# Kernel optimization log

Measured on AMD Instinct MI355X. Metric: run time of the kernel, lower is better.

## Reference

```python
import jax, jax.numpy as jnp
import numpy as np

B, R, L_, K_, U_, E = 16, 32, 64, 16, 4, 64  # batch, realizations, APs, users, antennas, embed dim
C2 = 2 * U_                                   # input_dim_2 == output_dim == 2U
EPS = 1e-5


def _uniform(key, shape, fan_out, fan_in):
    # matches torch init: U(-ini, ini) with ini = sqrt(3/(out*in))
    ini = float(np.sqrt(3.0 / (fan_out * fan_in)))
    return jax.random.uniform(key, shape, jnp.float32, -ini, ini)


def setup_inputs() -> dict:
    key = jax.random.key(0)
    ks = jax.random.split(key, 12)
    return {
        "Hhat_real": jax.random.normal(ks[0], (B, R, L_, K_, U_), jnp.float32),
        "Hhat_imag": jax.random.normal(ks[1], (B, R, L_, K_, U_), jnp.float32),
        # layer 0 (hidden, out=E) -- note P3/P5 exist in torch but are unused in forward
        "P1_0": _uniform(ks[2], (E, E), E, E),
        "P2_0": _uniform(ks[3], (E, E), E, E),
        "P4_0": _uniform(ks[4], (E, C2), E, C2),
        "g0": jnp.ones((E,), jnp.float32),
        "b0": jnp.zeros((E,), jnp.float32),
        # layer 1 (hidden, out=E)
        "P1_1": _uniform(ks[5], (E, E), E, E),
        "P2_1": _uniform(ks[6], (E, E), E, E),
        "P4_1": _uniform(ks[7], (E, C2), E, C2),
        "g1": jnp.ones((E,), jnp.float32),
        "b1": jnp.zeros((E,), jnp.float32),
        # layer 2 (output, out=2U, no BN / no ReLU)
        "P1_2": _uniform(ks[8], (C2, E), C2, E),
        "P2_2": _uniform(ks[9], (C2, E), C2, E),
        "P4_2": _uniform(ks[10], (C2, C2), C2, C2),
        "nbrOfRealizations": R,
        "L": L_,
        "K": K_,
        "U": U_,
    }


def _layer(A, H, P1, P2, P4, gamma, beta, is_last):
    # A: [BR, C1, L, K], H: [BR, C2, L, K]
    A1 = jnp.einsum('oc,bclk->bolk', P1, A)
    A2 = jnp.einsum('oc,bcl->bol', P2, A.mean(-1))[:, :, :, None]   # mean over K
    A3 = jnp.einsum('oc,bck->bok', P2, A.mean(-2))[:, :, None, :]   # mean over L
    A4 = jnp.einsum('oc,bcl->bol', P4, H.mean(-1))[:, :, :, None]
    A5 = jnp.einsum('oc,bck->bok', P4, H.mean(-2))[:, :, None, :]
    out = 2 * A1 + 2 * A2 + 2 * A3 + 0.1 * A4 + 0.1 * A5
    if is_last:
        return out
    out = jax.nn.relu(out)
    # BatchNorm2d, training mode: biased variance over (batch, L, K)
    mu = out.mean((0, 2, 3), keepdims=True)
    var = ((out - mu) ** 2).mean((0, 2, 3), keepdims=True)
    return (out - mu) / jnp.sqrt(var + EPS) * gamma[None, :, None, None] + beta[None, :, None, None]


def reference(Hhat_real, Hhat_imag, P1_0, P2_0, P4_0, g0, b0,
              P1_1, P2_1, P4_1, g1, b1, P1_2, P2_2, P4_2,
              nbrOfRealizations, L, K, U):
    batch = Hhat_real.shape[0]
    BR = batch * nbrOfRealizations
    # [B,R,L,K,U] -> [BR,U,L,K] (real / imag channels), concat -> [BR, 2U, L, K]
    Hr = Hhat_real.reshape(BR, L, K, U).transpose(0, 3, 1, 2)
    Hi = Hhat_imag.reshape(BR, L, K, U).transpose(0, 3, 1, 2)
    Hup = jnp.concatenate([Hr, Hi], axis=1)
    A = jnp.zeros((BR, E, L, K), jnp.float32)  # V_AP_updated init
    A = _layer(A, Hup, P1_0, P2_0, P4_0, g0, b0, False)
    A = _layer(A, Hup, P1_1, P2_1, P4_1, g1, b1, False)
    V = _layer(A, Hup, P1_2, P2_2, P4_2, None, None, True)  # [BR, 2U, L, K]
    V = V.reshape(BR, 2, U, L, K)
    F1 = jnp.transpose(V[:, 0], (0, 2, 3, 1))  # [BR, L, K, U]
    F2 = jnp.transpose(V[:, 1], (0, 2, 3, 1))
    norm = jnp.sqrt((F1 ** 2).sum(-1) + (F2 ** 2).sum(-1))[..., None]
    Fhat = (F1 + 1j * F2) / norm
    return Fhat.reshape(batch, nbrOfRealizations, L, K, U)
```

## Files before the change

kernel.cpp:

```cpp
#include <hip/hip_runtime.h>
#include <math.h>

#define BRR 512
#define LLL 64
#define KKK 16
#define EEE 64
#define CC2 8
#define PPP 1024
#define BN_EPS 1e-5f
#define NSTRIPE 16

__device__ __forceinline__ float relu_f(float v){ return v>0.f?v:0.f; }
__device__ __forceinline__ int lds_row(int r){ return r*68 + (((r>>3)&7)<<2); }

#define OFF_HBL  0u
#define OFF_HBK  262144u
#define OFF_Y0   327680u
#define OFF_X1   851968u
#define OFF_Y1   2949120u
#define OFF_X2   3473408u
#define OFF_Y2   3735552u
#define OFF_M1L  3801088u
#define OFF_M1K  5898240u
#define OFF_SUM0 6422528u
#define OFF_SSQ0 6423552u
#define OFF_SUM1 6424576u
#define OFF_SSQ1 6425600u
#define OFF_S0   6426624u
#define OFF_T0   6426688u
#define OFF_S1   6426752u
#define OFF_T1   6426816u
#define WS_FLOATS 6426880u
#define OFF_M1KB 6426880u
#define OFF_T1S  6951168u
#define WS_BIG   40505600u

__global__ void k_zero(float4* __restrict__ p, int n4){
  int t = blockIdx.x*256 + threadIdx.x;
  if (t < n4) p[t] = make_float4(0.f,0.f,0.f,0.f);
}

__global__ __launch_bounds__(256) void k_prep(const float* __restrict__ Hr,
                                              const float* __restrict__ Hi,
                                              const float* __restrict__ P40,
                                              float* __restrict__ ws){
  __shared__ float sm[9344];
  int b = blockIdx.x, tid = threadIdx.x;
  const float* hrg = Hr + (size_t)b*4096;
  const float* hig = Hi + (size_t)b*4096;
  for (int t=tid;t<4096;t+=256){ sm[t]=hrg[t]; sm[4096+t]=hig[t]; }
  for (int t=tid;t<512;t+=256){ int c=t&63,j=t>>6; sm[8192+j*64+c]=P40[c*8+j]; }
  __syncthreads();
  for (int t=tid;t<512;t+=256){ int l=t>>3,c2=t&7;
    const float* src=sm+((c2<4)?0:4096); int u=c2&3;
    float s=0.f;
    #pragma unroll
    for(int k=0;k<16;++k) s+=src[(l*16+k)*4+u];
    sm[8704+t]=s*(1.f/16.f); }
  for (int t=tid;t<128;t+=256){ int k=t>>3,c2=t&7;
    const float* src=sm+((c2<4)?0:4096); int u=c2&3;
    float s=0.f;
    for(int l=0;l<64;++l) s+=src[(l*16+k)*4+u];
    sm[9216+t]=s*(1.f/64.f); }
  __syncthreads();
  for (int t=tid;t<1024;t+=256){ int k=t>>6,c=t&63; float s=0.f;
    #pragma unroll
    for(int j=0;j<8;++j) s+=sm[8192+j*64+c]*sm[9216+k*8+j];
    sm[4096+t]=0.1f*s; }
  for (int t=tid;t<4096;t+=256){ int l=t>>6,c=t&63; float s=0.f;
    #pragma unroll
    for(int j=0;j<8;++j) s+=sm[8192+j*64+c]*sm[8704+l*8+j];
    sm[t]=0.1f*s; }
  __syncthreads();
  for (int t=tid;t<1024;t+=256){ int c=t&63; float yv=sm[4096+t]; float s=0.f;
    for(int l=0;l<64;++l) s+=relu_f(sm[l*64+c]+yv);
    sm[5120+t]=s*(1.f/64.f); }
  float ssum=0.f, ssq=0.f;
  for (int t=tid;t<4096;t+=256){ int c=t&63; float xv=sm[t]; float s=0.f;
    #pragma unroll
    for(int k=0;k<16;++k){ float v=relu_f(xv+sm[4096+k*64+c]); s+=v; ssq+=v*v; }
    ssum+=s;
    ws[OFF_X1+(size_t)b*4096+t]=s*(1.f/16.f); }
  __syncthreads();
  sm[6144+tid]=ssum; sm[6400+tid]=ssq;
  __syncthreads();
  if (tid<64){
    float ts =sm[6144+tid]+sm[6208+tid]+sm[6272+tid]+sm[6336+tid];
    float tss=sm[6400+tid]+sm[6464+tid]+sm[6528+tid]+sm[6592+tid];
    int stripe = b & (NSTRIPE-1);
    atomicAdd(&ws[OFF_SUM0+stripe*64+tid], ts);
    atomicAdd(&ws[OFF_SSQ0+stripe*64+tid], tss);
  }
  for (int t=tid;t<512;t+=256)  ws[OFF_HBL+(size_t)b*512+t]=sm[8704+t];
  for (int t=tid;t<128;t+=256)  ws[OFF_HBK+(size_t)b*128+t]=sm[9216+t];
  for (int t=tid;t<1024;t+=256) ws[OFF_Y0+(size_t)b*1024+t]=sm[4096+t];
  for (int t=tid;t<1024;t+=256) ws[OFF_Y1+(size_t)b*1024+t]=sm[5120+t];
  for (int t=tid;t<4096;t+=256) ws[OFF_M1L+(size_t)b*4096+t]=sm[t];
}

__global__ void k_bn(float* __restrict__ ws, const float* __restrict__ g_,
                     const float* __restrict__ b_, unsigned sumOff, unsigned outOff){
  int tid = threadIdx.x;
  if (tid < 64){
    float s=0.f, ss=0.f;
    for (int i=0;i<NSTRIPE;++i){ s+=ws[sumOff+i*64+tid]; ss+=ws[sumOff+1024+i*64+tid]; }
    const float invN = 1.0f/((float)BRR*LLL*KKK);
    float mu=s*invN, var=ss*invN-mu*mu;
    float sc = g_[tid]/sqrtf(var+BN_EPS);
    ws[outOff+tid]=sc;
    ws[outOff+64+tid]=b_[tid]-mu*sc;
  }
}

__global__ __launch_bounds__(256) void k_xy1(float* __restrict__ ws,
                                             const float* __restrict__ P21,
                                             const float* __restrict__ P41){
  __shared__ float wt[4096], p41[512], mrow[1024], hbs[128], s0l[64], t0l[64];
  int bx = blockIdx.x, tid = threadIdx.x;
  for (int t=tid;t<4096;t+=256) wt[t] = 2.0f*P21[(t&63)*64 + (t>>6)];
  for (int t=tid;t<512;t+=256)  p41[t] = P41[t];
  if (tid<64){ s0l[tid]=ws[OFF_S0+tid]; t0l[tid]=ws[OFF_T0+tid]; }
  bool isX = bx < 2048;
  int row0 = isX ? bx*16 : (bx-2048)*16;
  if (isX){
    for (int t=tid;t<1024;t+=256) mrow[t] = ws[OFF_X1+(size_t)row0*64+t];
    if (tid<128) hbs[tid] = ws[OFF_HBL+(size_t)row0*8+tid];
  } else {
    for (int t=tid;t<1024;t+=256) mrow[t] = ws[OFF_Y1+(size_t)row0*64+t];
    if (tid<128) hbs[tid] = ws[OFF_HBK+(size_t)row0*8+tid];
  }
  __syncthreads();
  for (int t=tid;t<1024;t+=256){ int c=t&63; mrow[t]=s0l[c]*mrow[t]+t0l[c]; }
  __syncthreads();
  int r4 = tid>>6, o = tid&63;
  #pragma unroll
  for (int rr=0;rr<4;++rr){
    int rl = rr*4 + r4;
    float s=0.f;
    for (int c=0;c<64;++c) s += wt[c*64+o]*mrow[rl*64+c];
    float s2=0.f;
    #pragma unroll
    for (int j=0;j<8;++j) s2 += p41[o*8+j]*hbs[rl*8+j];
    float res = s + 0.1f*s2;
    if (isX) ws[OFF_X1+(size_t)(row0+rl)*64+o] = res;
    else     ws[OFF_Y1+(size_t)(row0+rl)*64+o] = res;
  }
}

#define T_W1   0
#define T_X08  4384
#define T_Y0   4896
#define T_X1   5984
#define T_Y1   6496
#define T_S0   7520
#define T_T0   7584
#define T_P4T0 7648
#define T_HB8  8160
#define T_END  8224

__device__ void t1_tile(float* sm, const float* __restrict__ ws,
                        const float* __restrict__ P11, const float* __restrict__ P40,
                        int b, int pblk, int tid,
                        float acc[8][4], int og, int pg, int lloc, int c0){
  for (int t=tid;t<4096;t+=256){ int o=t>>6,c=t&63; sm[T_W1+lds_row(o)+c]=2.0f*P11[t]; }
  for (int t=tid;t<1024;t+=256){ int k=t>>6,c=t&63; sm[T_Y0+k*68+c]=ws[OFF_Y0+(size_t)b*1024+t]; }
  for (int t=tid;t<512;t+=256)  sm[T_X1+t]=ws[OFF_X1+((size_t)b*64+pblk*8)*64+t];
  for (int t=tid;t<1024;t+=256) sm[T_Y1+t]=ws[OFF_Y1+(size_t)b*1024+t];
  for (int t=tid;t<512;t+=256){ int c=t&63,j=t>>6; sm[T_P4T0+j*64+c]=P40[c*8+j]; }
  if (tid<64){ sm[T_S0+tid]=ws[OFF_S0+tid]; sm[T_T0+tid]=ws[OFF_T0+tid]; }
  else if (tid<128){ int t2=tid-64; sm[T_HB8+t2]=ws[OFF_HBL+((size_t)b*64+pblk*8)*8+t2]; }
  __syncthreads();
  for (int e=tid;e<512;e+=256){ int l=e>>6,c=e&63; float s=0.f;
    #pragma unroll
    for(int j=0;j<8;++j) s += sm[T_P4T0+j*64+c]*sm[T_HB8+l*8+j];
    sm[T_X08+e]=0.1f*s; }
  __syncthreads();
  {
    float xb[8];
    *(float4*)&xb[0] = *(const float4*)&sm[T_X1 + lloc*64 + c0];
    *(float4*)&xb[4] = *(const float4*)&sm[T_X1 + lloc*64 + c0 + 4];
    #pragma unroll
    for (int i=0;i<4;++i){
      int k=(pg&3)*4+i;
      float yb[8];
      *(float4*)&yb[0] = *(const float4*)&sm[T_Y1 + k*64 + c0];
      *(float4*)&yb[4] = *(const float4*)&sm[T_Y1 + k*64 + c0 + 4];
      #pragma unroll
      for (int j=0;j<8;++j) acc[j][i]=xb[j]+yb[j];
    }
  }
  #pragma unroll 4
  for (int c4=0;c4<16;++c4){
    float4 xr  = *(const float4*)&sm[T_X08 + lloc*64 + c4*4];
    float4 s0v = *(const float4*)&sm[T_S0 + c4*4];
    float4 t0v = *(const float4*)&sm[T_T0 + c4*4];
    float4 aa[4];
    #pragma unroll
    for (int i=0;i<4;++i){
      int k=(pg&3)*4+i;
      float4 yr = *(const float4*)&sm[T_Y0 + k*68 + c4*4];
      aa[i].x = s0v.x*relu_f(xr.x+yr.x)+t0v.x;
      aa[i].y = s0v.y*relu_f(xr.y+yr.y)+t0v.y;
      aa[i].z = s0v.z*relu_f(xr.z+yr.z)+t0v.z;
      aa[i].w = s0v.w*relu_f(xr.w+yr.w)+t0v.w;
    }
    #pragma unroll
    for (int j=0;j<8;++j){
      float4 w = *(const float4*)&sm[T_W1 + lds_row(c0+j) + c4*4];
      #pragma unroll
      for (int i=0;i<4;++i)
        acc[j][i] += w.x*aa[i].x + w.y*aa[i].y + w.z*aa[i].z + w.w*aa[i].w;
    }
  }
  #pragma unroll
  for (int j=0;j<8;++j)
    #pragma unroll
    for (int i=0;i<4;++i) acc[j][i] = relu_f(acc[j][i]);
}

#define PD_W1   0
#define PD_Y0   4384
#define PD_Y1   5472
#define PD_X1D  6496
#define PD_X08D 7520
#define PD_CT   8544
#define PD_S0   8608
#define PD_T0   8672
#define PD_TOT  8736

__global__ __launch_bounds__(256) void k_pass1f(float* __restrict__ ws,
                                                const float* __restrict__ P11){
  __shared__ float sm[PD_TOT];
  int b = blockIdx.x >> 1, h = blockIdx.x & 1;
  int pb0 = h*4;
  int tid=threadIdx.x;
  int og=tid&7, kg=(tid>>3)&3, lloc=tid>>5, c0=og*8, wv=tid>>6;
  for (int t4=tid;t4<1024;t4+=256){ int o=t4>>4,c=(t4&15)*4;
    float4 v = *(const float4*)&P11[o*64+c];
    v.x*=2.f; v.y*=2.f; v.z*=2.f; v.w*=2.f;
    *(float4*)&sm[PD_W1+lds_row(o)+c]=v; }
  for (int t4=tid;t4<256;t4+=256){
    float4 v = *(const float4*)&ws[OFF_Y0+(size_t)b*1024+t4*4];
    *(float4*)&sm[PD_Y0+(t4>>4)*68+((t4&15)*4)]=v; }
  for (int t4=tid;t4<256;t4+=256)
    *(float4*)&sm[PD_Y1+t4*4] = *(const float4*)&ws[OFF_Y1+(size_t)b*1024+t4*4];
  if (tid<64){ sm[PD_S0+tid]=ws[OFF_S0+tid]; sm[PD_T0+tid]=ws[OFF_T0+tid]; }
  {
    int po = tid>>7, idx = tid&127;
    float4 v1 = *(const float4*)&ws[OFF_X1 +((size_t)b*64+(pb0+po)*8)*64 + (size_t)idx*4];
    float4 v8 = *(const float4*)&ws[OFF_M1L+((size_t)b*64+(pb0+po)*8)*64 + (size_t)idx*4];
    *(float4*)&sm[PD_X1D  + po*512 + idx*4] = v1;
    *(float4*)&sm[PD_X08D + po*512 + idx*4] = v8;
  }
  __syncthreads();
  if (tid<64){
    float ct=0.f;
    for (int c=0;c<64;++c) ct += sm[PD_W1+lds_row(tid)+c]*sm[PD_T0+c];
    sm[PD_CT+tid]=ct;
  }
  __syncthreads();
  for (int t4=tid;t4<1024;t4+=256){ int o=t4>>4,c=(t4&15)*4;
    float4 w = *(float4*)&sm[PD_W1+lds_row(o)+c];
    float4 s = *(const float4*)&sm[PD_S0+c];
    w.x*=s.x; w.y*=s.y; w.z*=s.z; w.w*=s.w;
    *(float4*)&sm[PD_W1+lds_row(o)+c]=w; }
  float qsum[8], mk[8][4];
  #pragma unroll
  for (int j=0;j<8;++j){ qsum[j]=0.f;
    #pragma unroll
    for (int i=0;i<4;++i) mk[j][i]=0.f; }
  #pragma unroll 1
  for (int pr=0;pr<2;++pr){
    int pblkA = pb0 + 2*pr, pblkB = pblkA + 1;
    __syncthreads();
    float4 n1, n8;
    if (pr==0){
      int po = tid>>7, idx = tid&127, pn = pb0 + 2 + po;
      n1 = *(const float4*)&ws[OFF_X1 +((size_t)b*64+pn*8)*64 + (size_t)idx*4];
      n8 = *(const float4*)&ws[OFF_M1L+((size_t)b*64+pn*8)*64 + (size_t)idx*4];
    }
    float accA[8][4], accB[8][4];
    {
      float xbA[8], xbB[8], ctv[8];
      *(float4*)&xbA[0] = *(const float4*)&sm[PD_X1D       + lloc*64 + c0];
      *(float4*)&xbA[4] = *(const float4*)&sm[PD_X1D       + lloc*64 + c0 + 4];
      *(float4*)&xbB[0] = *(const float4*)&sm[PD_X1D + 512 + lloc*64 + c0];
      *(float4*)&xbB[4] = *(const float4*)&sm[PD_X1D + 512 + lloc*64 + c0 + 4];
      *(float4*)&ctv[0] = *(const float4*)&sm[PD_CT + c0];
      *(float4*)&ctv[4] = *(const float4*)&sm[PD_CT + c0 + 4];
      #pragma unroll
      for (int i=0;i<4;++i){
        int k=kg*4+i;
        float yb[8];
        *(float4*)&yb[0] = *(const float4*)&sm[PD_Y1 + k*64 + c0];
        *(float4*)&yb[4] = *(const float4*)&sm[PD_Y1 + k*64 + c0 + 4];
        #pragma unroll
        for (int j=0;j<8;++j){
          float base = yb[j]+ctv[j];
          accA[j][i]=xbA[j]+base;
          accB[j][i]=xbB[j]+base;
        }
      }
    }
    #pragma unroll 2
    for (int c4=0;c4<16;++c4){
      float4 xrA = *(const float4*)&sm[PD_X08D       + lloc*64 + c4*4];
      float4 xrB = *(const float4*)&sm[PD_X08D + 512 + lloc*64 + c4*4];
      float4 aaA[4], aaB[4];
      #pragma unroll
      for (int i=0;i<4;++i){
        int k=kg*4+i;
        float4 yr = *(const float4*)&sm[PD_Y0 + k*68 + c4*4];
        aaA[i].x = relu_f(xrA.x+yr.x); aaB[i].x = relu_f(xrB.x+yr.x);
        aaA[i].y = relu_f(xrA.y+yr.y); aaB[i].y = relu_f(xrB.y+yr.y);
        aaA[i].z = relu_f(xrA.z+yr.z); aaB[i].z = relu_f(xrB.z+yr.z);
        aaA[i].w = relu_f(xrA.w+yr.w); aaB[i].w = relu_f(xrB.w+yr.w);
      }
      #pragma unroll
      for (int j=0;j<8;++j){
        float4 w = *(const float4*)&sm[PD_W1 + lds_row(c0+j) + c4*4];
        #pragma unroll
        for (int i=0;i<4;++i){
          accA[j][i] += w.x*aaA[i].x + w.y*aaA[i].y + w.z*aaA[i].z + w.w*aaA[i].w;
          accB[j][i] += w.x*aaB[i].x + w.y*aaB[i].y + w.z*aaB[i].z + w.w*aaB[i].w;
        }
      }
    }
    #pragma unroll
    for (int j=0;j<8;++j)
      #pragma unroll
      for (int i=0;i<4;++i){
        accA[j][i] = relu_f(accA[j][i]);
        accB[j][i] = relu_f(accB[j][i]);
      }
    {
      size_t tbA = OFF_T1S + ((size_t)b*8 + pblkA)*8192 + (size_t)tid*4;
      size_t tbB = OFF_T1S + ((size_t)b*8 + pblkB)*8192 + (size_t)tid*4;
      #pragma unroll
      for (int j=0;j<8;++j){
        *(float4*)&ws[tbA + j*1024] =
          make_float4(accA[j][0],accA[j][1],accA[j][2],accA[j][3]);
        *(float4*)&ws[tbB + j*1024] =
          make_float4(accB[j][0],accB[j][1],accB[j][2],accB[j][3]);
      }
    }
    float sjA[8], sjB[8];
    #pragma unroll
    for (int j=0;j<8;++j){
      sjA[j]=accA[j][0]+accA[j][1]+accA[j][2]+accA[j][3];
      sjB[j]=accB[j][0]+accB[j][1]+accB[j][2]+accB[j][3];
      qsum[j]+=accA[j][0]*accA[j][0]+accA[j][1]*accA[j][1]+accA[j][2]*accA[j][2]+accA[j][3]*accA[j][3];
      qsum[j]+=accB[j][0]*accB[j][0]+accB[j][1]*accB[j][1]+accB[j][2]*accB[j][2]+accB[j][3]*accB[j][3];
      #pragma unroll
      for (int i=0;i<4;++i) mk[j][i]+=accA[j][i]+accB[j][i];
    }
    #pragma unroll
    for (int j=0;j<8;++j){
      float rA=sjA[j];
      rA += __shfl_xor(rA, 8, 64);
      rA += __shfl_xor(rA, 16, 64);
      sjA[j]=rA;
      float rB=sjB[j];
      rB += __shfl_xor(rB, 8, 64);
      rB += __shfl_xor(rB, 16, 64);
      sjB[j]=rB;
    }
    if (kg==0){
      const float inv16 = 1.f/16.f;
      size_t baseA = OFF_M1L + ((size_t)b*64 + pblkA*8 + lloc)*64 + c0;
      size_t baseB = OFF_M1L + ((size_t)b*64 + pblkB*8 + lloc)*64 + c0;
      *(float4*)&ws[baseA]   = make_float4(sjA[0]*inv16, sjA[1]*inv16, sjA[2]*inv16, sjA[3]*inv16);
      *(float4*)&ws[baseA+4] = make_float4(sjA[4]*inv16, sjA[5]*inv16, sjA[6]*inv16, sjA[7]*inv16);
      *(float4*)&ws[baseB]   = make_float4(sjB[0]*inv16, sjB[1]*inv16, sjB[2]*inv16, sjB[3]*inv16);
      *(float4*)&ws[baseB+4] = make_float4(sjB[4]*inv16, sjB[5]*inv16, sjB[6]*inv16, sjB[7]*inv16);
    }
    if (pr==0){
      __syncthreads();
      int po = tid>>7, idx = tid&127;
      *(float4*)&sm[PD_X1D  + po*512 + idx*4] = n1;
      *(float4*)&sm[PD_X08D + po*512 + idx*4] = n8;
    }
  }
  __syncthreads();
  #pragma unroll
  for (int j=0;j<8;++j){
    #pragma unroll
    for (int i=0;i<4;++i){
      float v = mk[j][i] + __shfl_xor(mk[j][i], 32, 64);
      if ((tid & 32)==0)
        sm[wv*1088 + (og*4+kg)*33 + i*8 + j] = v;
    }
  }
  {
    int pg = tid>>3;
    #pragma unroll
    for (int j=0;j<8;++j) sm[4384+(c0+j)*33+pg] = qsum[j];
  }
  __syncthreads();
  unsigned mko = h ? OFF_M1KB : OFF_M1K;
  float tsacc=0.f;
  #pragma unroll
  for (int r=0;r<4;++r){
    int e = tid + r*256;
    int k=e>>6, c=e&63;
    int a = ((c>>3)*4+(k>>2))*33 + (k&3)*8 + (c&7);
    float v = sm[a]+sm[1088+a]+sm[2176+a]+sm[3264+a];
    tsacc += v;
    ws[mko+(size_t)b*1024+e] = v*(1.f/64.f);
  }
  sm[6496 + (tid&63)*5 + wv] = tsacc;
  __syncthreads();
  if (tid<64){
    float ts  = sm[6496+tid*5+0]+sm[6496+tid*5+1]+sm[6496+tid*5+2]+sm[6496+tid*5+3];
    float tss = 0.f;
    for (int g=0; g<32; ++g) tss += sm[4384+tid*33+g];
    int stripe = b & (NSTRIPE-1);
    atomicAdd(&ws[OFF_SUM1+stripe*64+tid], ts);
    atomicAdd(&ws[OFF_SSQ1+stripe*64+tid], tss);
  }
}

#define MK_OFF 8224
__global__ __launch_bounds__(256) void k_pass1(float* __restrict__ ws,
                                               const float* __restrict__ P11,
                                               const float* __restrict__ P40){
  __shared__ float sm[12576];
  int b=blockIdx.x, tid=threadIdx.x;
  int og=tid&7, pg=tid>>3, lloc=pg>>2, kg=pg&3, c0=og*8, wv=tid>>6;
  for (int t=tid;t<4096;t+=256){ int o=t>>6,c=t&63; sm[T_W1+lds_row(o)+c]=2.0f*P11[t]; }
  for (int t=tid;t<1024;t+=256){ int k=t>>6,c=t&63; sm[T_Y0+k*68+c]=ws[OFF_Y0+(size_t)b*1024+t]; }
  for (int t=tid;t<1024;t+=256) sm[T_Y1+t]=ws[OFF_Y1+(size_t)b*1024+t];
  for (int t=tid;t<512;t+=256){ int c=t&63,j=t>>6; sm[T_P4T0+j*64+c]=P40[c*8+j]; }
  if (tid<64){ sm[T_S0+tid]=ws[OFF_S0+tid]; sm[T_T0+tid]=ws[OFF_T0+tid]; }
  for (int t=tid;t<4352;t+=256) sm[MK_OFF+t]=0.f;
  float qsum[8];
  #pragma unroll
  for (int j=0;j<8;++j) qsum[j]=0.f;
  #pragma unroll 1
  for (int pblk=0;pblk<8;++pblk){
    __syncthreads();
    for (int t=tid;t<512;t+=256) sm[T_X1+t]=ws[OFF_X1+((size_t)b*64+pblk*8)*64+t];
    if (tid<64) sm[T_HB8+tid]=ws[OFF_HBL+((size_t)b*64+pblk*8)*8+tid];
    __syncthreads();
    for (int e=tid;e<512;e+=256){ int l=e>>6,c=e&63; float s=0.f;
      #pragma unroll
      for(int j=0;j<8;++j) s += sm[T_P4T0+j*64+c]*sm[T_HB8+l*8+j];
      sm[T_X08+e]=0.1f*s; }
    __syncthreads();
    float acc[8][4];
    {
      float xb[8];
      *(float4*)&xb[0] = *(const float4*)&sm[T_X1 + lloc*64 + c0];
      *(float4*)&xb[4] = *(const float4*)&sm[T_X1 + lloc*64 + c0 + 4];
      #pragma unroll
      for (int i=0;i<4;++i){
        int k=kg*4+i;
        float yb[8];
        *(float4*)&yb[0] = *(const float4*)&sm[T_Y1 + k*64 + c0];
        *(float4*)&yb[4] = *(const float4*)&sm[T_Y1 + k*64 + c0 + 4];
        #pragma unroll
        for (int j=0;j<8;++j) acc[j][i]=xb[j]+yb[j];
      }
    }
    #pragma unroll 4
    for (int c4=0;c4<16;++c4){
      float4 xr  = *(const float4*)&sm[T_X08 + lloc*64 + c4*4];
      float4 s0v = *(const float4*)&sm[T_S0 + c4*4];
      float4 t0v = *(const float4*)&sm[T_T0 + c4*4];
      float4 aa[4];
      #pragma unroll
      for (int i=0;i<4;++i){
        int k=kg*4+i;
        float4 yr = *(const float4*)&sm[T_Y0 + k*68 + c4*4];
        aa[i].x = s0v.x*relu_f(xr.x+yr.x)+t0v.x;
        aa[i].y = s0v.y*relu_f(xr.y+yr.y)+t0v.y;
        aa[i].z = s0v.z*relu_f(xr.z+yr.z)+t0v.z;
        aa[i].w = s0v.w*relu_f(xr.w+yr.w)+t0v.w;
      }
      #pragma unroll
      for (int j=0;j<8;++j){
        float4 w = *(const float4*)&sm[T_W1 + lds_row(c0+j) + c4*4];
        #pragma unroll
        for (int i=0;i<4;++i)
          acc[j][i] += w.x*aa[i].x + w.y*aa[i].y + w.z*aa[i].z + w.w*aa[i].w;
      }
    }
    #pragma unroll
    for (int j=0;j<8;++j)
      #pragma unroll
      for (int i=0;i<4;++i) acc[j][i] = relu_f(acc[j][i]);
    float sj[8];
    #pragma unroll
    for (int j=0;j<8;++j){
      sj[j]=acc[j][0]+acc[j][1]+acc[j][2]+acc[j][3];
      qsum[j]+=acc[j][0]*acc[j][0]+acc[j][1]*acc[j][1]+acc[j][2]*acc[j][2]+acc[j][3]*acc[j][3];
    }
    #pragma unroll
    for (int j=0;j<8;++j){
      float r=sj[j];
      r += __shfl_xor(r, 8, 64);
      r += __shfl_xor(r, 16, 64);
      sj[j]=r;
    }
    if (kg==0){
      const float inv16 = 1.f/16.f;
      float4 v0 = make_float4(sj[0]*inv16, sj[1]*inv16, sj[2]*inv16, sj[3]*inv16);
      float4 v1 = make_float4(sj[4]*inv16, sj[5]*inv16, sj[6]*inv16, sj[7]*inv16);
      size_t base = OFF_M1L + ((size_t)b*64 + pblk*8 + lloc)*64 + c0;
      *(float4*)&ws[base]   = v0;
      *(float4*)&ws[base+4] = v1;
    }
    #pragma unroll
    for (int j=0;j<8;++j){
      #pragma unroll
      for (int i=0;i<4;++i){
        float v = acc[j][i] + __shfl_xor(acc[j][i], 32, 64);
        if ((tid & 32)==0)
          sm[MK_OFF + wv*1088 + (og*4+kg)*33 + i*8 + j] += v;
      }
    }
  }
  __syncthreads();
  float tsacc=0.f;
  #pragma unroll
  for (int r=0;r<4;++r){
    int e = tid + r*256;
    int k=e>>6, c=e&63;
    int a = ((c>>3)*4+(k>>2))*33 + (k&3)*8 + (c&7);
    float v = sm[MK_OFF+a]+sm[MK_OFF+1088+a]+sm[MK_OFF+2176+a]+sm[MK_OFF+3264+a];
    tsacc += v;
    ws[OFF_M1K+(size_t)b*1024+e] = v*(1.f/64.f);
  }
  __syncthreads();
  sm[8224 + (tid&63)*5 + wv] = tsacc;
  #pragma unroll
  for (int j=0;j<8;++j) sm[8544+(c0+j)*33+pg] = qsum[j];
  __syncthreads();
  if (tid<64){
    float ts  = sm[8224+tid*5+0]+sm[8224+tid*5+1]+sm[8224+tid*5+2]+sm[8224+tid*5+3];
    float tss = 0.f;
    for (int g=0; g<32; ++g) tss += sm[8544+tid*33+g];
    int stripe = b & (NSTRIPE-1);
    atomicAdd(&ws[OFF_SUM1+stripe*64+tid], ts);
    atomicAdd(&ws[OFF_SSQ1+stripe*64+tid], tss);
  }
}

__global__ __launch_bounds__(256) void k_xy2s(float* __restrict__ ws,
                                              const float* __restrict__ P22,
                                              const float* __restrict__ P42,
                                              int two){
  __shared__ float mln[4352];
  __shared__ float mkn[1088];
  __shared__ float w2[512];
  __shared__ float p42s[64];
  __shared__ float hbl[512];
  __shared__ float hbk[128];
  __shared__ float s1l[64], t1l[64];
  int b = blockIdx.x, tid = threadIdx.x;
  if (tid<64){ s1l[tid]=ws[OFF_S1+tid]; t1l[tid]=ws[OFF_T1+tid]; }
  for (int t=tid;t<512;t+=256) w2[t] = 2.0f*P22[(t&7)*64 + (t>>3)];
  if (tid<64) p42s[tid] = P42[tid];
  for (int t=tid;t<512;t+=256) hbl[t] = ws[OFF_HBL+(size_t)b*512+t];
  if (tid<128) hbk[tid] = ws[OFF_HBK+(size_t)b*128+tid];
  __syncthreads();
  for (int t=tid;t<4096;t+=256){ int l=t>>6,c=t&63;
    mln[l*68+c] = s1l[c]*ws[OFF_M1L+(size_t)b*4096+t] + t1l[c]; }
  for (int t=tid;t<1024;t+=256){ int k=t>>6,c=t&63;
    float mv = ws[OFF_M1K+(size_t)b*1024+t];
    if (two) mv += ws[OFF_M1KB+(size_t)b*1024+t];
    mkn[k*68+c] = s1l[c]*mv + t1l[c]; }
  __syncthreads();
  for (int t=tid;t<512;t+=256){
    int l=t>>3, o2=t&7;
    float s=0.f;
    for (int c=0;c<64;++c) s += w2[c*8+o2]*mln[l*68+c];
    float s2=0.f;
    #pragma unroll
    for (int j=0;j<8;++j) s2 += p42s[o2*8+j]*hbl[l*8+j];
    ws[OFF_X2+(size_t)b*512+t] = s + 0.1f*s2;
  }
  if (tid<128){
    int k=tid>>3, o2=tid&7;
    float s=0.f;
    for (int c=0;c<64;++c) s += w2[c*8+o2]*mkn[k*68+c];
    float s2=0.f;
    #pragma unroll
    for (int j=0;j<8;++j) s2 += p42s[o2*8+j]*hbk[k*8+j];
    ws[OFF_Y2+(size_t)b*128+tid] = s + 0.1f*s2;
  }
}

__device__ __forceinline__ void final_epilogue(const float* __restrict__ ws,
                                               float* sm, int b, int pblk, int tid,
                                               float* __restrict__ out,
                                               long long out_cap, int interleaved){
  if (tid < 128){
    int p = tid, k = p & 15, lglob = pblk*8 + (p>>4);
    float a2[8];
    {
      const float* xp = ws + OFF_X2 + ((size_t)b*64+lglob)*8;
      const float* yp = ws + OFF_Y2 + ((size_t)b*16+k)*8;
      float4 x0_ = *(const float4*)&xp[0];
      float4 x1_ = *(const float4*)&xp[4];
      float4 y0_ = *(const float4*)&yp[0];
      float4 y1_ = *(const float4*)&yp[4];
      a2[0]=x0_.x+y0_.x; a2[1]=x0_.y+y0_.y; a2[2]=x0_.z+y0_.z; a2[3]=x0_.w+y0_.w;
      a2[4]=x1_.x+y1_.x; a2[5]=x1_.y+y1_.y; a2[6]=x1_.z+y1_.z; a2[7]=x1_.w+y1_.w;
    }
    for (int c=0;c<64;++c){
      float tn = sm[9028+c]*sm[c*133 + (c>>3) + p] + sm[9092+c];
      #pragma unroll
      for (int o2=0;o2<8;++o2) a2[o2] += sm[8516+o2*64+c]*tn;
    }
    float nrm=0.f;
    #pragma unroll
    for (int o2=0;o2<8;++o2) nrm += a2[o2]*a2[o2];
    float inv = 1.0f/sqrtf(nrm);
    size_t pos = (size_t)b*PPP + lglob*KKK + k;
    if (interleaved){
      long long idx = (long long)pos*8;
      if (idx+8 <= out_cap){
        *(float4*)&out[idx]   = make_float4(a2[0]*inv, a2[4]*inv, a2[1]*inv, a2[5]*inv);
        *(float4*)&out[idx+4] = make_float4(a2[2]*inv, a2[6]*inv, a2[3]*inv, a2[7]*inv);
      }
    } else {
      long long idx = (long long)pos*4;
      if (idx+4 <= out_cap)
        *(float4*)&out[idx] = make_float4(a2[0]*inv, a2[1]*inv, a2[2]*inv, a2[3]*inv);
    }
  }
}

__global__ __launch_bounds__(256) void k_final_big(const float* __restrict__ ws,
                                                   const float* __restrict__ P12,
                                                   float* __restrict__ out,
                                                   long long out_cap, int interleaved){
  __shared__ float sm[9156];
  int bid=blockIdx.x, b=bid>>3, pblk=bid&7, tid=threadIdx.x;
  for (int t=tid;t<512;t+=256) sm[8516+t] = 2.0f*P12[t];
  if (tid<64) sm[9028+tid]=ws[OFF_S1+tid];
  else if (tid<128) sm[9092+(tid-64)]=ws[OFF_T1+(tid-64)];
  {
    size_t base = OFF_T1S + ((size_t)b*8 + pblk)*8192;
    for (int t4=tid;t4<2048;t4+=256){
      float4 v = *(const float4*)&ws[base + (size_t)t4*4];
      int j = t4>>8, lane = t4&255;
      int c = (lane&7)*8 + j;
      int pb = (lane>>5)*16 + ((lane>>3)&3)*4;
      int o = c*133 + (c>>3) + pb;
      sm[o+0]=v.x; sm[o+1]=v.y; sm[o+2]=v.z; sm[o+3]=v.w;
    }
  }
  __syncthreads();
  int half = tid>>7, p = tid&127;
  int k = p & 15, lglob = pblk*8 + (p>>4);
  float a2[8];
  if (half==0){
    const float* xp = ws + OFF_X2 + ((size_t)b*64+lglob)*8;
    const float* yp = ws + OFF_Y2 + ((size_t)b*16+k)*8;
    float4 x0_ = *(const float4*)&xp[0];
    float4 x1_ = *(const float4*)&xp[4];
    float4 y0_ = *(const float4*)&yp[0];
    float4 y1_ = *(const float4*)&yp[4];
    a2[0]=x0_.x+y0_.x; a2[1]=x0_.y+y0_.y; a2[2]=x0_.z+y0_.z; a2[3]=x0_.w+y0_.w;
    a2[4]=x1_.x+y1_.x; a2[5]=x1_.y+y1_.y; a2[6]=x1_.z+y1_.z; a2[7]=x1_.w+y1_.w;
  } else {
    #pragma unroll
    for (int o2=0;o2<8;++o2) a2[o2]=0.f;
  }
  int cb = half*32;
  for (int cc=0;cc<32;++cc){
    int c = cb+cc;
    float tn = sm[9028+c]*sm[c*133 + (c>>3) + p] + sm[9092+c];
    #pragma unroll
    for (int o2=0;o2<8;++o2) a2[o2] += sm[8516+o2*64+c]*tn;
  }
  __syncthreads();
  if (half==1){
    #pragma unroll
    for (int o2=0;o2<8;++o2) sm[p*9+o2] = a2[o2];
  }
  __syncthreads();
  if (half==0){
    #pragma unroll
    for (int o2=0;o2<8;++o2) a2[o2] += sm[p*9+o2];
    float nrm=0.f;
    #pragma unroll
    for (int o2=0;o2<8;++o2) nrm += a2[o2]*a2[o2];
    float inv = 1.0f/sqrtf(nrm);
    size_t pos = (size_t)b*PPP + lglob*KKK + k;
    if (interleaved){
      long long idx = (long long)pos*8;
      if (idx+8 <= out_cap){
        *(float4*)&out[idx]   = make_float4(a2[0]*inv, a2[4]*inv, a2[1]*inv, a2[5]*inv);
        *(float4*)&out[idx+4] = make_float4(a2[2]*inv, a2[6]*inv, a2[3]*inv, a2[7]*inv);
      }
    } else {
      long long idx = (long long)pos*4;
      if (idx+4 <= out_cap)
        *(float4*)&out[idx] = make_float4(a2[0]*inv, a2[1]*inv, a2[2]*inv, a2[3]*inv);
    }
  }
}

__global__ __launch_bounds__(256) void k_final(const float* __restrict__ ws,
                                               const float* __restrict__ P11,
                                               const float* __restrict__ P40,
                                               const float* __restrict__ P12,
                                               float* __restrict__ out,
                                               long long out_cap, int interleaved){
  __shared__ float sm[9156];
  int bid=blockIdx.x, b=bid>>3, pblk=bid&7, tid=threadIdx.x;
  int og=tid&7, pg=tid>>3, lloc=pg>>2, c0=og*8;
  for (int t=tid;t<512;t+=256) sm[8516+t] = 2.0f*P12[t];
  if (tid<64) sm[9028+tid]=ws[OFF_S1+tid];
  else if (tid<128) sm[9092+(tid-64)]=ws[OFF_T1+(tid-64)];
  float acc[8][4];
  t1_tile(sm, ws, P11, P40, b, pblk, tid, acc, og, pg, lloc, c0);
  __syncthreads();
  {
    int kg = pg&3;
    #pragma unroll
    for (int i=0;i<4;++i){
      int p = lloc*16 + kg*4 + i;
      #pragma unroll
      for (int j=0;j<8;++j) sm[(c0+j)*133 + og + p] = acc[j][i];
    }
  }
  __syncthreads();
  final_epilogue(ws, sm, b, pblk, tid, out, out_cap, interleaved);
}

extern "C" void kernel_launch(void* const* d_in, const int* in_sizes, int n_in,
                              void* d_out, int out_size, void* d_ws, size_t ws_size,
                              hipStream_t stream) {
  if (n_in < 15) return;
  if (in_sizes[0] != BRR*4096 || in_sizes[1] != BRR*4096) return;
  if (in_sizes[4] != 512)  return;
  if (in_sizes[7] != 4096) return;
  if (in_sizes[12] != 512) return;
  if (ws_size < (size_t)WS_FLOATS*4) return;

  const float* Hr   = (const float*)d_in[0];
  const float* Hi   = (const float*)d_in[1];
  const float* P4_0 = (const float*)d_in[4];
  const float* g0   = (const float*)d_in[5];
  const float* b0   = (const float*)d_in[6];
  const float* P1_1 = (const float*)d_in[7];
  const float* P2_1 = (const float*)d_in[8];
  const float* P4_1 = (const float*)d_in[9];
  const float* g1   = (const float*)d_in[10];
  const float* b1   = (const float*)d_in[11];
  const float* P1_2 = (const float*)d_in[12];
  const float* P2_2 = (const float*)d_in[13];
  const float* P4_2 = (const float*)d_in[14];
  float* ws  = (float*)d_ws;
  float* out = (float*)d_out;
  int interleaved = (out_size >= 4194304) ? 1 : 0;
  int big = (ws_size >= (size_t)WS_BIG*4) ? 1 : 0;

  k_zero<<<4, 256, 0, stream>>>((float4*)(ws + OFF_SUM0), 4096/4);
  k_prep<<<BRR, 256, 0, stream>>>(Hr, Hi, P4_0, ws);
  k_bn<<<1, 64, 0, stream>>>(ws, g0, b0, OFF_SUM0, OFF_S0);
  k_xy1<<<2560, 256, 0, stream>>>(ws, P2_1, P4_1);
  if (big) k_pass1f<<<BRR*2, 256, 0, stream>>>(ws, P1_1);
  else     k_pass1<<<BRR, 256, 0, stream>>>(ws, P1_1, P4_0);
  k_bn<<<1, 64, 0, stream>>>(ws, g1, b1, OFF_SUM1, OFF_S1);
  k_xy2s<<<BRR, 256, 0, stream>>>(ws, P2_2, P4_2, big);
  if (big) k_final_big<<<BRR*8, 256, 0, stream>>>(ws, P1_2, out,
                                                  (long long)out_size, interleaved);
  else     k_final<<<BRR*8, 256, 0, stream>>>(ws, P1_1, P4_0, P1_2, out,
                                              (long long)out_size, interleaved);
}
```

Before: 284.5 us.

## Fold BatchNorm finalize into consumer kernels and vectorize global/LDS copies

Removes the two single-block k_bn launches on the big-workspace path: each consumer block now recomputes the BN scale and shift from the striped sum and sum-of-squares buffers. Several scalar copy loops become float4, and the transposed P2_1 weight in k_xy1 gets a 65-float row pitch to avoid LDS bank conflicts. The trade is redundant per-block reads of the 2048-float stat buffers (thousands of blocks) in exchange for fewer launches and serial gaps. The loads of p42s and hbk in k_xy2s move to other thread ranges to overlap with the BN work.

```diff
diff --git a/kernel.cpp b/kernel.cpp
--- a/kernel.cpp
+++ b/kernel.cpp
@@ -35,6 +35,22 @@
 #define OFF_T1S  6951168u
 #define WS_BIG   40505600u
 
+__device__ __forceinline__ void bn_inline(const float* __restrict__ ws,
+                                          unsigned sumOff,
+                                          const float* __restrict__ g_,
+                                          const float* __restrict__ b_,
+                                          int tid, float* sc_out, float* st_out){
+  if (tid < 64){
+    float s=0.f, ss=0.f;
+    for (int i=0;i<NSTRIPE;++i){ s+=ws[sumOff+i*64+tid]; ss+=ws[sumOff+1024+i*64+tid]; }
+    const float invN = 1.0f/((float)BRR*LLL*KKK);
+    float mu=s*invN, var=ss*invN-mu*mu;
+    float sc = g_[tid]/sqrtf(var+BN_EPS);
+    sc_out[tid]=sc;
+    st_out[tid]=b_[tid]-mu*sc;
+  }
+}
+
 __global__ void k_zero(float4* __restrict__ p, int n4){
   int t = blockIdx.x*256 + threadIdx.x;
   if (t < n4) p[t] = make_float4(0.f,0.f,0.f,0.f);
@@ -48,7 +64,10 @@
   int b = blockIdx.x, tid = threadIdx.x;
   const float* hrg = Hr + (size_t)b*4096;
   const float* hig = Hi + (size_t)b*4096;
-  for (int t=tid;t<4096;t+=256){ sm[t]=hrg[t]; sm[4096+t]=hig[t]; }
+  for (int t4=tid;t4<1024;t4+=256){
+    *(float4*)&sm[t4*4]      = *(const float4*)&hrg[t4*4];
+    *(float4*)&sm[4096+t4*4] = *(const float4*)&hig[t4*4];
+  }
   for (int t=tid;t<512;t+=256){ int c=t&63,j=t>>6; sm[8192+j*64+c]=P40[c*8+j]; }
   __syncthreads();
   for (int t=tid;t<512;t+=256){ int l=t>>3,c2=t&7;
@@ -91,42 +110,47 @@
     atomicAdd(&ws[OFF_SUM0+stripe*64+tid], ts);
     atomicAdd(&ws[OFF_SSQ0+stripe*64+tid], tss);
   }
-  for (int t=tid;t<512;t+=256)  ws[OFF_HBL+(size_t)b*512+t]=sm[8704+t];
+  for (int t4=tid;t4<128;t4+=256)
+    *(float4*)&ws[OFF_HBL+(size_t)b*512+t4*4] = *(const float4*)&sm[8704+t4*4];
   for (int t=tid;t<128;t+=256)  ws[OFF_HBK+(size_t)b*128+t]=sm[9216+t];
-  for (int t=tid;t<1024;t+=256) ws[OFF_Y0+(size_t)b*1024+t]=sm[4096+t];
-  for (int t=tid;t<1024;t+=256) ws[OFF_Y1+(size_t)b*1024+t]=sm[5120+t];
-  for (int t=tid;t<4096;t+=256) ws[OFF_M1L+(size_t)b*4096+t]=sm[t];
+  for (int t4=tid;t4<256;t4+=256)
+    *(float4*)&ws[OFF_Y0+(size_t)b*1024+t4*4] = *(const float4*)&sm[4096+t4*4];
+  for (int t4=tid;t4<256;t4+=256)
+    *(float4*)&ws[OFF_Y1+(size_t)b*1024+t4*4] = *(const float4*)&sm[5120+t4*4];
+  for (int t4=tid;t4<1024;t4+=256)
+    *(float4*)&ws[OFF_M1L+(size_t)b*4096+t4*4] = *(const float4*)&sm[t4*4];
 }
 
 __global__ void k_bn(float* __restrict__ ws, const float* __restrict__ g_,
                      const float* __restrict__ b_, unsigned sumOff, unsigned outOff){
   int tid = threadIdx.x;
-  if (tid < 64){
-    float s=0.f, ss=0.f;
-    for (int i=0;i<NSTRIPE;++i){ s+=ws[sumOff+i*64+tid]; ss+=ws[sumOff+1024+i*64+tid]; }
-    const float invN = 1.0f/((float)BRR*LLL*KKK);
-    float mu=s*invN, var=ss*invN-mu*mu;
-    float sc = g_[tid]/sqrtf(var+BN_EPS);
-    ws[outOff+tid]=sc;
-    ws[outOff+64+tid]=b_[tid]-mu*sc;
-  }
+  bn_inline(ws, sumOff, g_, b_, tid, ws+outOff, ws+outOff+64);
 }
 
 __global__ __launch_bounds__(256) void k_xy1(float* __restrict__ ws,
                                              const float* __restrict__ P21,
-                                             const float* __restrict__ P41){
-  __shared__ float wt[4096], p41[512], mrow[1024], hbs[128], s0l[64], t0l[64];
+                                             const float* __restrict__ P41,
+                                             const float* __restrict__ g0,
+                                             const float* __restrict__ b0){
+  __shared__ float wt[4160], p41[512], mrow[1024], hbs[128], s0l[64], t0l[64];
   int bx = blockIdx.x, tid = threadIdx.x;
-  for (int t=tid;t<4096;t+=256) wt[t] = 2.0f*P21[(t&63)*64 + (t>>6)];
+  for (int t4=tid;t4<1024;t4+=256){
+    int o=t4>>4, c4=(t4&15)*4;
+    float4 v = *(const float4*)&P21[o*64+c4];
+    wt[(c4+0)*65+o]=2.f*v.x; wt[(c4+1)*65+o]=2.f*v.y;
+    wt[(c4+2)*65+o]=2.f*v.z; wt[(c4+3)*65+o]=2.f*v.w;
+  }
   for (int t=tid;t<512;t+=256)  p41[t] = P41[t];
-  if (tid<64){ s0l[tid]=ws[OFF_S0+tid]; t0l[tid]=ws[OFF_T0+tid]; }
+  bn_inline(ws, OFF_SUM0, g0, b0, tid, s0l, t0l);
   bool isX = bx < 2048;
   int row0 = isX ? bx*16 : (bx-2048)*16;
   if (isX){
-    for (int t=tid;t<1024;t+=256) mrow[t] = ws[OFF_X1+(size_t)row0*64+t];
+    for (int t4=tid;t4<256;t4+=256)
+      *(float4*)&mrow[t4*4] = *(const float4*)&ws[OFF_X1+(size_t)row0*64+t4*4];
     if (tid<128) hbs[tid] = ws[OFF_HBL+(size_t)row0*8+tid];
   } else {
-    for (int t=tid;t<1024;t+=256) mrow[t] = ws[OFF_Y1+(size_t)row0*64+t];
+    for (int t4=tid;t4<256;t4+=256)
+      *(float4*)&mrow[t4*4] = *(const float4*)&ws[OFF_Y1+(size_t)row0*64+t4*4];
     if (tid<128) hbs[tid] = ws[OFF_HBK+(size_t)row0*8+tid];
   }
   __syncthreads();
@@ -137,7 +161,7 @@
   for (int rr=0;rr<4;++rr){
     int rl = rr*4 + r4;
     float s=0.f;
-    for (int c=0;c<64;++c) s += wt[c*64+o]*mrow[rl*64+c];
+    for (int c=0;c<64;++c) s += wt[c*65+o]*mrow[rl*64+c];
     float s2=0.f;
     #pragma unroll
     for (int j=0;j<8;++j) s2 += p41[o*8+j]*hbs[rl*8+j];
@@ -229,7 +253,9 @@
 #define PD_TOT  8736
 
 __global__ __launch_bounds__(256) void k_pass1f(float* __restrict__ ws,
-                                                const float* __restrict__ P11){
+                                                const float* __restrict__ P11,
+                                                const float* __restrict__ g0,
+                                                const float* __restrict__ b0){
   __shared__ float sm[PD_TOT];
   int b = blockIdx.x >> 1, h = blockIdx.x & 1;
   int pb0 = h*4;
@@ -244,7 +270,7 @@
     *(float4*)&sm[PD_Y0+(t4>>4)*68+((t4&15)*4)]=v; }
   for (int t4=tid;t4<256;t4+=256)
     *(float4*)&sm[PD_Y1+t4*4] = *(const float4*)&ws[OFF_Y1+(size_t)b*1024+t4*4];
-  if (tid<64){ sm[PD_S0+tid]=ws[OFF_S0+tid]; sm[PD_T0+tid]=ws[OFF_T0+tid]; }
+  bn_inline(ws, OFF_SUM0, g0, b0, tid, sm+PD_S0, sm+PD_T0);
   {
     int po = tid>>7, idx = tid&127;
     float4 v1 = *(const float4*)&ws[OFF_X1 +((size_t)b*64+(pb0+po)*8)*64 + (size_t)idx*4];
@@ -549,6 +575,8 @@
 __global__ __launch_bounds__(256) void k_xy2s(float* __restrict__ ws,
                                               const float* __restrict__ P22,
                                               const float* __restrict__ P42,
+                                              const float* __restrict__ g1,
+                                              const float* __restrict__ b1,
                                               int two){
   __shared__ float mln[4352];
   __shared__ float mkn[1088];
@@ -558,11 +586,11 @@
   __shared__ float hbk[128];
   __shared__ float s1l[64], t1l[64];
   int b = blockIdx.x, tid = threadIdx.x;
-  if (tid<64){ s1l[tid]=ws[OFF_S1+tid]; t1l[tid]=ws[OFF_T1+tid]; }
+  bn_inline(ws, OFF_SUM1, g1, b1, tid, s1l, t1l);
   for (int t=tid;t<512;t+=256) w2[t] = 2.0f*P22[(t&7)*64 + (t>>3)];
-  if (tid<64) p42s[tid] = P42[tid];
+  if (tid>=64 && tid<128) p42s[tid-64] = P42[tid-64];
   for (int t=tid;t<512;t+=256) hbl[t] = ws[OFF_HBL+(size_t)b*512+t];
-  if (tid<128) hbk[tid] = ws[OFF_HBK+(size_t)b*128+tid];
+  if (tid>=128 && tid<256 && tid-128<128) hbk[tid-128] = ws[OFF_HBK+(size_t)b*128+(tid-128)];
   __syncthreads();
   for (int t=tid;t<4096;t+=256){ int l=t>>6,c=t&63;
     mln[l*68+c] = s1l[c]*ws[OFF_M1L+(size_t)b*4096+t] + t1l[c]; }
@@ -634,13 +662,14 @@
 
 __global__ __launch_bounds__(256) void k_final_big(const float* __restrict__ ws,
                                                    const float* __restrict__ P12,
+                                                   const float* __restrict__ g1,
+                                                   const float* __restrict__ b1,
                                                    float* __restrict__ out,
                                                    long long out_cap, int interleaved){
   __shared__ float sm[9156];
   int bid=blockIdx.x, b=bid>>3, pblk=bid&7, tid=threadIdx.x;
   for (int t=tid;t<512;t+=256) sm[8516+t] = 2.0f*P12[t];
-  if (tid<64) sm[9028+tid]=ws[OFF_S1+tid];
-  else if (tid<128) sm[9092+(tid-64)]=ws[OFF_T1+(tid-64)];
+  bn_inline(ws, OFF_SUM1, g1, b1, tid, sm+9028, sm+9092);
   {
     size_t base = OFF_T1S + ((size_t)b*8 + pblk)*8192;
     for (int t4=tid;t4<2048;t4+=256){
@@ -762,14 +791,19 @@
 
   k_zero<<<4, 256, 0, stream>>>((float4*)(ws + OFF_SUM0), 4096/4);
   k_prep<<<BRR, 256, 0, stream>>>(Hr, Hi, P4_0, ws);
-  k_bn<<<1, 64, 0, stream>>>(ws, g0, b0, OFF_SUM0, OFF_S0);
-  k_xy1<<<2560, 256, 0, stream>>>(ws, P2_1, P4_1);
-  if (big) k_pass1f<<<BRR*2, 256, 0, stream>>>(ws, P1_1);
-  else     k_pass1<<<BRR, 256, 0, stream>>>(ws, P1_1, P4_0);
-  k_bn<<<1, 64, 0, stream>>>(ws, g1, b1, OFF_SUM1, OFF_S1);
-  k_xy2s<<<BRR, 256, 0, stream>>>(ws, P2_2, P4_2, big);
-  if (big) k_final_big<<<BRR*8, 256, 0, stream>>>(ws, P1_2, out,
-                                                  (long long)out_size, interleaved);
-  else     k_final<<<BRR*8, 256, 0, stream>>>(ws, P1_1, P4_0, P1_2, out,
-                                              (long long)out_size, interleaved);
-}
+  if (big){
+    k_xy1<<<2560, 256, 0, stream>>>(ws, P2_1, P4_1, g0, b0);
+    k_pass1f<<<BRR*2, 256, 0, stream>>>(ws, P1_1, g0, b0);
+    k_xy2s<<<BRR, 256, 0, stream>>>(ws, P2_2, P4_2, g1, b1, 1);
+    k_final_big<<<BRR*8, 256, 0, stream>>>(ws, P1_2, g1, b1, out,
+                                           (long long)out_size, interleaved);
+  } else {
+    k_bn<<<1, 64, 0, stream>>>(ws, g0, b0, OFF_SUM0, OFF_S0);
+    k_xy1<<<2560, 256, 0, stream>>>(ws, P2_1, P4_1, g0, b0);
+    k_pass1<<<BRR, 256, 0, stream>>>(ws, P1_1, P4_0);
+    k_bn<<<1, 64, 0, stream>>>(ws, g1, b1, OFF_SUM1, OFF_S1);
+    k_xy2s<<<BRR, 256, 0, stream>>>(ws, P2_2, P4_2, g1, b1, 0);
+    k_final<<<BRR*8, 256, 0, stream>>>(ws, P1_1, P4_0, P1_2, out,
+                                       (long long)out_size, interleaved);
+  }
+}
```

Result: faster. 273.6 us, median of 2 (-3.8%).
